# Optimization experiments

Measured on AMD Instinct MI355X. Metric: run time of the kernel, lower is better.

Reference implementation:

```python
import jax, jax.numpy as jnp
from jax import lax
import numpy as np

INPUT_DIM = 1024; ENT_DIM = 256; KEY_DIM = 32; FUNC_DIM = 256; HID = 32
NUM_LAYERS = 1; UNIT_TYPE_DIM = 259; MAX_ENT = 64; B = 256; N = 512
NEG = 1e9

def _ln(x, g, b, eps=1e-5):
    m = x.mean(-1, keepdims=True)
    v = ((x - m) ** 2).mean(-1, keepdims=True)
    return (x - m) / jnp.sqrt(v + eps) * g + b

def setup_inputs() -> dict:
    key = jax.random.key(0)
    ks = jax.random.split(key, 16)
    def lin(k, i, o, s=0.02):
        return jax.random.normal(k, (i, o), jnp.float32) * s, jnp.zeros((o,), jnp.float32)
    p = {}
    p['key_fc_w'], p['key_fc_b'] = lin(ks[0], ENT_DIM, KEY_DIM)
    p['func_fc_w'], p['func_fc_b'] = lin(ks[1], UNIT_TYPE_DIM, FUNC_DIM)
    p['fc1_w'], p['fc1_b'] = lin(ks[2], INPUT_DIM, FUNC_DIM)
    p['fc2_w'], p['fc2_b'] = lin(ks[3], FUNC_DIM, KEY_DIM)
    p['embed_fc_w'], p['embed_fc_b'] = lin(ks[4], KEY_DIM, INPUT_DIM)
    p['lstm_wx'] = jax.random.normal(ks[5], (NUM_LAYERS, KEY_DIM, 4 * HID), jnp.float32) * 0.05
    p['lstm_wh'] = jax.random.normal(ks[6], (NUM_LAYERS, HID, 4 * HID), jnp.float32) * 0.05
    p['lstm_b'] = jnp.zeros((NUM_LAYERS, 4 * HID), jnp.float32)
    p['lstm_ln_gx'] = jnp.ones((NUM_LAYERS, 4 * HID), jnp.float32)
    p['lstm_ln_bx'] = jnp.zeros((NUM_LAYERS, 4 * HID), jnp.float32)
    p['lstm_ln_gh'] = jnp.ones((NUM_LAYERS, 4 * HID), jnp.float32)
    p['lstm_ln_bh'] = jnp.zeros((NUM_LAYERS, 4 * HID), jnp.float32)
    inp = {
        'embedding': jax.random.normal(ks[7], (B, INPUT_DIM), jnp.float32),
        'available_unit_type_mask': (jax.random.uniform(ks[8], (B, UNIT_TYPE_DIM)) < 0.5).astype(jnp.float32),
        'available_units_mask': jnp.ones((B, N), jnp.float32),
        'entity_embedding': jax.random.normal(ks[9], (B, N, ENT_DIM), jnp.float32),
        'temperature': jnp.float32(1.0),
    }
    inp.update(p)
    return inp

def reference(embedding, available_unit_type_mask, available_units_mask, entity_embedding,
              temperature, key_fc_w, key_fc_b, func_fc_w, func_fc_b, fc1_w, fc1_b,
              fc2_w, fc2_b, embed_fc_w, embed_fc_b, lstm_wx, lstm_wh, lstm_b,
              lstm_ln_gx, lstm_ln_bx, lstm_ln_gh, lstm_ln_bh):
    relu = jax.nn.relu
    # _get_key: [B,N,KEY] + end-flag row of zeros -> [B,N+1,KEY]
    key = entity_embedding @ key_fc_w + key_fc_b
    key = jnp.concatenate([key, jnp.zeros((B, 1, KEY_DIM), key.dtype)], axis=1)
    end_idx = N
    # _get_init_query
    func_embed = relu(available_unit_type_mask @ func_fc_w + func_fc_b)
    x0 = relu(embedding @ fc1_w + fc1_b)
    x0 = relu((x0 + func_embed) @ fc2_w + fc2_b)  # [B, KEY_DIM]
    mask0 = jnp.concatenate([available_units_mask, jnp.ones((B, 1), available_units_mask.dtype)], axis=1)

    h0 = jnp.zeros((NUM_LAYERS, B, HID), key.dtype)
    c0 = jnp.zeros((NUM_LAYERS, B, HID), key.dtype)
    units0 = jnp.zeros((B, N + 1), jnp.int32)
    done0 = jnp.zeros((B,), bool)
    rng0 = jax.random.key(42)

    def step(carry, _):
        x, h, c, mask, units, done, rng = carry
        xi = x
        hs, cs = [], []
        for l in range(NUM_LAYERS):  # LN-LSTM, gate order i,f,o,u (DI-engine)
            gate = (_ln(xi @ lstm_wx[l], lstm_ln_gx[l], lstm_ln_bx[l])
                    + _ln(h[l] @ lstm_wh[l], lstm_ln_gh[l], lstm_ln_bh[l]) + lstm_b[l])
            i_g, f_g, o_g, u_g = jnp.split(gate, 4, axis=-1)
            cl = jax.nn.sigmoid(f_g) * c[l] + jax.nn.sigmoid(i_g) * jnp.tanh(u_g)
            hl = jax.nn.sigmoid(o_g) * jnp.tanh(cl)
            hs.append(hl); cs.append(cl); xi = hl
        h_new = jnp.stack(hs); c_new = jnp.stack(cs)
        q = (xi[:, None, :] * key).mean(-1)          # [B, N+1] pointer scores
        q = q - (1.0 - mask) * NEG
        rng, sk = jax.random.split(rng)
        idx = jax.random.categorical(sk, q / temperature, axis=-1)  # [B]
        is_end = idx == end_idx
        active = jnp.logical_not(done)
        sel = active & jnp.logical_not(is_end)
        onehot = jax.nn.one_hot(idx, N + 1, dtype=mask.dtype)
        units = jnp.where(sel[:, None] & (onehot > 0.5), 1, units)
        mask = jnp.where(sel[:, None], mask * (1.0 - onehot), mask)
        done = done | (active & is_end)
        return (xi, h_new, c_new, mask, units, done, rng), (q, active)

    carry, (logits, valid) = lax.scan(step, (x0, h0, c0, mask0, units0, done0, rng0), None, length=MAX_ENT)
    units = carry[4]
    emb_sel = (units[..., None].astype(key.dtype) * key).mean(axis=1)  # [B, KEY_DIM]
    emb_sel = emb_sel @ embed_fc_w + embed_fc_b
    return logits, valid, units, embedding + emb_sel
```

## Files before the change

### kernel.cpp

```cpp
#include <hip/hip_runtime.h>
#include <stdint.h>
#include <stddef.h>

#define JAX_PARTITIONABLE 1

#define B_   256
#define N_   512
#define NP_  513
#define KROW 516
#define T_   64
#define CS   4
#define NCH  16
#define NEGC 1e9f

__host__ __device__ __forceinline__ void tf2x32(uint32_t k0, uint32_t k1,
    uint32_t x0, uint32_t x1, uint32_t& o0, uint32_t& o1) {
  const uint32_t k2 = k0 ^ k1 ^ 0x1BD11BDAu;
#define TFR(r) { x0 += x1; x1 = (x1 << (r)) | (x1 >> (32 - (r))); x1 ^= x0; }
  x0 += k0; x1 += k1;
  TFR(13) TFR(15) TFR(26) TFR(6)
  x0 += k1; x1 += k2 + 1u;
  TFR(17) TFR(29) TFR(16) TFR(24)
  x0 += k2; x1 += k0 + 2u;
  TFR(13) TFR(15) TFR(26) TFR(6)
  x0 += k0; x1 += k1 + 3u;
  TFR(17) TFR(29) TFR(16) TFR(24)
  x0 += k1; x1 += k2 + 4u;
  TFR(13) TFR(15) TFR(26) TFR(6)
  x0 += k2; x1 += k0 + 5u;
#undef TFR
  o0 = x0; o1 = x1;
}

struct SkKeys { uint32_t k[128]; };

static SkKeys compute_chain() {
  SkKeys s;
  uint32_t r0 = 0u, r1 = 42u;
  for (int t = 0; t < 64; ++t) {
#if JAX_PARTITIONABLE
    uint32_t a0, a1, b0, b1;
    tf2x32(r0, r1, 0u, 0u, a0, a1);
    tf2x32(r0, r1, 0u, 1u, b0, b1);
    s.k[2*t] = b0; s.k[2*t+1] = b1;
    r0 = a0; r1 = a1;
#else
    uint32_t p0, p1, q0, q1;
    tf2x32(r0, r1, 0u, 2u, p0, p1);
    tf2x32(r0, r1, 1u, 3u, q0, q1);
    s.k[2*t] = p1; s.k[2*t+1] = q1;
    r0 = p0; r1 = q0;
#endif
  }
  return s;
}

__device__ __forceinline__ float gumbel_draw(uint32_t k0, uint32_t k1, int b, int n) {
  uint32_t bits;
#if JAX_PARTITIONABLE
  uint32_t j = (uint32_t)(b * NP_ + n);
  uint32_t o0, o1; tf2x32(k0, k1, 0u, j, o0, o1);
  bits = o0 ^ o1;
#else
  int j = b * NP_ + n;
  uint32_t o0, o1;
  if (j < 65664) { tf2x32(k0, k1, (uint32_t)j, (uint32_t)(j + 65664), o0, o1); bits = o0; }
  else           { tf2x32(k0, k1, (uint32_t)(j - 65664), (uint32_t)j, o0, o1); bits = o1; }
#endif
  float f = __uint_as_float((bits >> 9) | 0x3F800000u) - 1.0f;
  const float TINY = 1.17549435e-38f;
  float u = fmaxf(TINY, f + TINY);
  return -logf(-logf(u));
}

__device__ __forceinline__ float sigm(float x) {
  return 0.5f + 0.5f * tanhf(0.5f * x);
}

__device__ __forceinline__ void bar_lds() {
  asm volatile("s_waitcnt lgkmcnt(0)\n\ts_barrier" ::: "memory");
}

#define WS_KEY 0
#define WS_X0  (B_ * 32 * KROW)

__global__ void __launch_bounds__(256)
pre_kernel(const float* __restrict__ ent, const float* __restrict__ key_w,
           const float* __restrict__ key_b,
           const float* __restrict__ emb, const float* __restrict__ fc1_w,
           const float* __restrict__ fc1_b,
           const float* __restrict__ autm, const float* __restrict__ func_w,
           const float* __restrict__ func_b,
           const float* __restrict__ fc2_w, const float* __restrict__ fc2_b,
           float* __restrict__ ws)
{
  __shared__ __align__(16) float smAll[16384];
  const int tid = threadIdx.x;

  if (blockIdx.x < 1024) {
    float* smA = smAll;
    float* smW = smAll + 8192;
    const int blk = blockIdx.x;
    const int R0  = blk * 128;
    const int b   = R0 >> 9;
    const int nb  = R0 & 511;
    const int rg  = tid >> 3;
    const int cg  = tid & 7;

    for (int i = tid; i < 2048; i += 256)
      ((float4*)smW)[i] = ((const float4*)key_w)[i];

    float acc[4][4];
    #pragma unroll
    for (int i = 0; i < 4; ++i)
      #pragma unroll
      for (int j = 0; j < 4; ++j) acc[i][j] = 0.f;

    const int row  = tid >> 1;
    const int half = tid & 1;

    for (int kc = 0; kc < 4; ++kc) {
      const float4* src = (const float4*)(ent + ((size_t)(R0 + row)) * 256 + kc * 64 + half * 32);
      float4 vv[8];
      #pragma unroll
      for (int r = 0; r < 8; ++r) vv[r] = src[r];
      #pragma unroll
      for (int r = 0; r < 8; ++r) {
        const int kl = half * 32 + r * 4;
        smA[(kl + 0) * 128 + row] = vv[r].x;
        smA[(kl + 1) * 128 + row] = vv[r].y;
        smA[(kl + 2) * 128 + row] = vv[r].z;
        smA[(kl + 3) * 128 + row] = vv[r].w;
      }
      __syncthreads();
      #pragma unroll 4
      for (int k = 0; k < 64; ++k) {
        float4 av = *(const float4*)&smA[k * 128 + rg * 4];
        float4 bv = *(const float4*)&smW[(kc * 64 + k) * 32 + cg * 4];
        float ar[4] = {av.x, av.y, av.z, av.w};
        float br[4] = {bv.x, bv.y, bv.z, bv.w};
        #pragma unroll
        for (int i = 0; i < 4; ++i)
          #pragma unroll
          for (int j = 0; j < 4; ++j) acc[i][j] += ar[i] * br[j];
      }
      __syncthreads();
    }
    float4 bb = *(const float4*)&key_b[cg * 4];
    float bbr[4] = {bb.x, bb.y, bb.z, bb.w};
    #pragma unroll
    for (int j = 0; j < 4; ++j) {
      const int c = cg * 4 + j;
      float* dst = ws + WS_KEY + ((size_t)(b * 32 + c)) * KROW + nb + rg * 4;
      #pragma unroll
      for (int i = 0; i < 4; ++i) dst[i] = acc[i][j] + bbr[j];
    }
  } else {
    float* smX = smAll;
    const int b = blockIdx.x - 1024;
    const int j = tid;
    {
      float a = 0.f;
      const float* e = emb + (size_t)b * 1024;
      #pragma unroll 8
      for (int k = 0; k < 1024; ++k) a += e[k] * fc1_w[k * 256 + j];
      a = fmaxf(a + fc1_b[j], 0.f);
      float f = 0.f;
      const float* m = autm + (size_t)b * 259;
      for (int k = 0; k < 259; ++k) f += m[k] * func_w[k * 256 + j];
      f = fmaxf(f + func_b[j], 0.f);
      smX[j] = a + f;
    }
    __syncthreads();
    if (j < 32) {
      float s = 0.f;
      #pragma unroll 8
      for (int m = 0; m < 256; ++m) s += smX[m] * fc2_w[m * 32 + j];
      ws[WS_X0 + b * 32 + j] = fmaxf(s + fc2_b[j], 0.f);
    }
  }
}

#define OFF_KEY   0
#define OFF_H     16512
#define OFF_Q     18560
#define OFF_G     22688
#define OFF_UNITS 26816
#define OFF_SK    27332
#define OFF_ES    27460
#define OFF_PART  27492
#define LDS_FLOATS 28004

__global__ void __launch_bounds__(512, 2)
suh_kernel(const float* __restrict__ ws_key_x0,
           const float* __restrict__ aum, const float* __restrict__ temp_p,
           const float* __restrict__ emb,
           const float* __restrict__ emb_w, const float* __restrict__ emb_b,
           const float* __restrict__ wx, const float* __restrict__ wh,
           const float* __restrict__ lstm_bb,
           const float* __restrict__ ln_gx, const float* __restrict__ ln_bx,
           const float* __restrict__ ln_gh, const float* __restrict__ ln_bh,
           float* __restrict__ out_logits, float* __restrict__ out_valid,
           float* __restrict__ out_units, float* __restrict__ out_final,
           SkKeys sk)
{
  extern __shared__ __align__(16) float sm[];
  int* smi = (int*)sm;
  const int b   = blockIdx.x;
  const int tid = threadIdx.x;

  {
    const float4* kv = (const float4*)(ws_key_x0 + WS_KEY + (size_t)b * (32 * KROW));
    for (int i = tid; i < (32 * KROW) / 4; i += 512) ((float4*)sm)[i] = kv[i];
  }
  if (tid < 128) smi[OFF_SK + tid] = (int)sk.k[tid];
  __syncthreads();
  if (tid < 32) sm[OFF_KEY + tid * KROW + N_] = 0.f;

  const float temp = temp_p[0];

  float mreg[8], ureg[8];
  float m512 = 1.0f;
  int done_reg = 0;

  if (tid < 64) {
    float wxr0[32], wxr1[32], whr0[32], whr1[32];
    #pragma unroll
    for (int k = 0; k < 32; ++k) {
      wxr0[k] = wx[k * 128 + tid];
      wxr1[k] = wx[k * 128 + 64 + tid];
      whr0[k] = wh[k * 128 + tid];
      whr1[k] = wh[k * 128 + 64 + tid];
    }
    const float gxg0 = ln_gx[tid], gxg1 = ln_gx[tid + 64];
    const float gxb0 = ln_bx[tid], gxb1 = ln_bx[tid + 64];
    const float ghg0 = ln_gh[tid], ghg1 = ln_gh[tid + 64];
    const float ghb0 = ln_bh[tid], ghb1 = ln_bh[tid + 64];
    const float lb0  = lstm_bb[tid], lb1 = lstm_bb[tid + 64];

    float xfrag[32];
    {
      const float* x0g = ws_key_x0 + WS_X0 + b * 32;
      #pragma unroll
      for (int r = 0; r < 8; ++r) {
        float4 v = *(const float4*)(x0g + r * 4);
        xfrag[r*4] = v.x; xfrag[r*4+1] = v.y; xfrag[r*4+2] = v.z; xfrag[r*4+3] = v.w;
      }
    }
    float creg = 0.f;

    #pragma unroll 1
    for (int t = 0; t < T_; ++t) {
      float a0 = 0.f, a1 = 0.f, b0 = 0.f, b1 = 0.f;
      #pragma unroll
      for (int k = 0; k < 32; ++k) {
        a0 += xfrag[k] * wxr0[k];
        a1 += xfrag[k] * wxr1[k];
      }
      if (t > 0) {
        #pragma unroll
        for (int k = 0; k < 32; ++k) {
          b0 += xfrag[k] * whr0[k];
          b1 += xfrag[k] * whr1[k];
        }
      }
      float sx = a0 + a1, sh = b0 + b1;
      for (int off = 32; off; off >>= 1) {
        sx += __shfl_down(sx, off);
        sh += __shfl_down(sh, off);
      }
      float mx  = __shfl(sx, 0) * (1.0f / 128.0f);
      float mhh = __shfl(sh, 0) * (1.0f / 128.0f);
      float dx0 = a0 - mx, dx1 = a1 - mx;
      float dh0 = b0 - mhh, dh1 = b1 - mhh;
      float ssx = dx0 * dx0 + dx1 * dx1;
      float ssh = dh0 * dh0 + dh1 * dh1;
      for (int off = 32; off; off >>= 1) {
        ssx += __shfl_down(ssx, off);
        ssh += __shfl_down(ssh, off);
      }
      float vx = __shfl(ssx, 0) * (1.0f / 128.0f);
      float vh = __shfl(ssh, 0) * (1.0f / 128.0f);
      float rx = 1.0f / sqrtf(vx + 1e-5f);
      float rh = 1.0f / sqrtf(vh + 1e-5f);
      float lnx0 = dx0 * rx * gxg0 + gxb0;
      float lnx1 = dx1 * rx * gxg1 + gxb1;
      float lnh0 = dh0 * rh * ghg0 + ghb0;
      float lnh1 = dh1 * rh * ghg1 + ghb1;
      float g0 = lnx0 + lnh0 + lb0;
      float g1 = lnx1 + lnh1 + lb1;
      float fq = __shfl(g0, tid + 32);
      float uq = __shfl(g1, tid + 32);
      if (tid < 32) {
        float cN = sigm(fq) * creg + sigm(g0) * tanhf(uq);
        float hN = sigm(g1) * tanhf(cN);
        creg = cN;
        sm[OFF_H + t * 32 + tid] = hN;
      }
      #pragma unroll
      for (int r = 0; r < 8; ++r) {
        float4 v = *(const float4*)&sm[OFF_H + t * 32 + r * 4];
        xfrag[r*4] = v.x; xfrag[r*4+1] = v.y; xfrag[r*4+2] = v.z; xfrag[r*4+3] = v.w;
      }
    }
  }
  __syncthreads();

  auto do_prep = [&](int cc, int pbuf) {
    const int L = tid - 64;
    const int qb = OFF_Q + pbuf * (CS * 516);
    const int gb = OFF_G + pbuf * (CS * 516);
    #pragma unroll 1
    for (int pass = 0; pass < 2; ++pass) {
      const int n = L + pass * 448;
      if (pass == 0 || L < 65) {
        float kreg[32];
        #pragma unroll
        for (int k = 0; k < 32; ++k) kreg[k] = sm[OFF_KEY + k * KROW + n];
        #pragma unroll
        for (int tl = 0; tl < CS; ++tl) {
          float acc = 0.f;
          #pragma unroll
          for (int k = 0; k < 32; ++k) acc += sm[OFF_H + (cc * CS + tl) * 32 + k] * kreg[k];
          sm[qb + tl * 516 + n] = acc * (1.0f / 32.0f);
        }
      }
    }
    #pragma unroll 1
    for (int i = 0; i < (CS * 512 + 447) / 448; ++i) {
      const int idx = i * 448 + L;
      if (idx < CS * 512) {
        const int tl = idx >> 9;
        const int n  = idx & 511;
        const int t  = cc * CS + tl;
        sm[gb + tl * 516 + n] =
            gumbel_draw((uint32_t)smi[OFF_SK + 2*t], (uint32_t)smi[OFF_SK + 2*t + 1], b, n);
      }
    }
    if (L < CS) {
      const int t = cc * CS + L;
      sm[gb + L * 516 + N_] =
          gumbel_draw((uint32_t)smi[OFF_SK + 2*t], (uint32_t)smi[OFF_SK + 2*t + 1], b, N_);
    }
  };

  if (tid >= 64) {
    do_prep(0, 0);
  } else {
    #pragma unroll
    for (int j = 0; j < 8; ++j) {
      const int n = tid + 64 * j;
      mreg[j] = aum[(size_t)b * N_ + n];
      ureg[j] = 0.f;
    }
  }
  bar_lds();

  for (int c = 0; c < NCH; ++c) {
    const int pb = c & 1;
    if (tid < 64) {
      const int qbase = OFF_Q + pb * (CS * 516);
      const int gbase = OFF_G + pb * (CS * 516);
      #pragma unroll 1
      for (int tl = 0; tl < CS; ++tl) {
        const int t = c * CS + tl;
        float* lrow = out_logits + ((size_t)t * B_ + b) * NP_;
        float bv = 0.f; int bi = 0;
        #pragma unroll
        for (int j = 0; j < 8; ++j) {
          const int n = tid + 64 * j;
          float q = sm[qbase + tl * 516 + n] - (1.0f - mreg[j]) * NEGC;
          lrow[n] = q;
          float v = q / temp + sm[gbase + tl * 516 + n];
          if (j == 0) { bv = v; bi = n; }
          else if (v > bv) { bv = v; bi = n; }
        }
        if (tid == 0) {
          float q = -(1.0f - m512) * NEGC;
          lrow[N_] = q;
          float v = q / temp + sm[gbase + tl * 516 + N_];
          if (v > bv) { bv = v; bi = N_; }
        }
        for (int off = 32; off; off >>= 1) {
          float ov = __shfl_down(bv, off);
          int   oi = __shfl_down(bi, off);
          if (ov > bv || (ov == bv && oi < bi)) { bv = ov; bi = oi; }
        }
        const int sel_i = __shfl(bi, 0);
        const int active = !done_reg;
        const int is_end = (sel_i == N_);
        if (tid == 0) out_valid[(size_t)t * B_ + b] = active ? 1.0f : 0.0f;
        if (active && !is_end) {
          #pragma unroll
          for (int j = 0; j < 8; ++j)
            if (tid + 64 * j == sel_i) { mreg[j] = 0.0f; ureg[j] = 1.0f; }
        }
        if (active && is_end) done_reg = 1;
      }
    } else if (c + 1 < NCH) {
      do_prep(c + 1, (c + 1) & 1);
    }
    bar_lds();
  }

  if (tid < 64) {
    #pragma unroll
    for (int j = 0; j < 8; ++j) sm[OFF_UNITS + tid + 64 * j] = ureg[j];
    if (tid == 0) sm[OFF_UNITS + N_] = 0.f;
  }
  __syncthreads();

  {
    const int g = tid >> 5, cc = tid & 31;
    float p = 0.f;
    const int n0 = g * 32;
    for (int nn = 0; nn < 32; ++nn) {
      const int n = n0 + nn;
      p += sm[OFF_UNITS + n] * sm[OFF_KEY + cc * KROW + n];
    }
    if (g == 15) p += sm[OFF_UNITS + N_] * sm[OFF_KEY + cc * KROW + N_];
    sm[OFF_PART + g * 32 + cc] = p;
  }
  for (int n = tid; n < NP_; n += 512) out_units[(size_t)b * NP_ + n] = sm[OFF_UNITS + n];
  __syncthreads();
  if (tid < 32) {
    float s = 0.f;
    #pragma unroll
    for (int g = 0; g < 16; ++g) s += sm[OFF_PART + g * 32 + tid];
    sm[OFF_ES + tid] = s / 513.0f;
  }
  __syncthreads();
  {
    const float* e = emb + (size_t)b * 1024;
    for (int d = tid; d < 1024; d += 512) {
      float a = 0.f;
      #pragma unroll
      for (int k = 0; k < 32; ++k) a += sm[OFF_ES + k] * emb_w[k * 1024 + d];
      out_final[(size_t)b * 1024 + d] = e[d] + a + emb_b[d];
    }
  }
}

extern "C" void kernel_launch(void* const* d_in, const int* in_sizes, int n_in,
                              void* d_out, int out_size, void* d_ws, size_t ws_size,
                              hipStream_t stream) {
  (void)in_sizes; (void)n_in; (void)ws_size; (void)out_size;
  const float* emb    = (const float*)d_in[0];
  const float* autm   = (const float*)d_in[1];
  const float* aum    = (const float*)d_in[2];
  const float* ent    = (const float*)d_in[3];
  const float* temp   = (const float*)d_in[4];
  const float* key_w  = (const float*)d_in[5];
  const float* key_b  = (const float*)d_in[6];
  const float* func_w = (const float*)d_in[7];
  const float* func_b = (const float*)d_in[8];
  const float* fc1_w  = (const float*)d_in[9];
  const float* fc1_b  = (const float*)d_in[10];
  const float* fc2_w  = (const float*)d_in[11];
  const float* fc2_b  = (const float*)d_in[12];
  const float* emb_w  = (const float*)d_in[13];
  const float* emb_b  = (const float*)d_in[14];
  const float* wx     = (const float*)d_in[15];
  const float* wh     = (const float*)d_in[16];
  const float* lb     = (const float*)d_in[17];
  const float* gxg    = (const float*)d_in[18];
  const float* gxb    = (const float*)d_in[19];
  const float* ghg    = (const float*)d_in[20];
  const float* ghb    = (const float*)d_in[21];
  float* out = (float*)d_out;
  float* ws  = (float*)d_ws;

  const size_t OFF_V = (size_t)T_ * B_ * NP_;
  const size_t OFF_U = OFF_V + (size_t)T_ * B_;
  const size_t OFF_F = OFF_U + (size_t)B_ * NP_;

  SkKeys sk = compute_chain();

  pre_kernel<<<dim3(1280), dim3(256), 0, stream>>>(
      ent, key_w, key_b, emb, fc1_w, fc1_b, autm, func_w, func_b,
      fc2_w, fc2_b, ws);

  suh_kernel<<<dim3(B_), dim3(512), LDS_FLOATS * sizeof(float), stream>>>(
      ws, aum, temp, emb, emb_w, emb_b,
      wx, wh, lb, gxg, gxb, ghg, ghb,
      out, out + OFF_V, out + OFF_U, out + OFF_F, sk);
}
```

Measured before the change: 275.4 us.

## Fuse key projection and MLP prologue into single per-batch pointer kernel

Removes the separate pre_kernel and computes the entity key projection, fc1/func/fc2 MLP and x0 inside the main per-batch kernel, overlapping the key GEMM with the LSTM recurrence on the first 64 threads. Each prep thread keeps its key columns in registers (kr0/kr1) so q computation reads h from LDS instead of reloading keys, and gumbel buffers are expanded to five slots so draws are prefetched several chunks ahead. The LSTM now broadcasts h via shuffles instead of an LDS round trip. It drops the workspace round trip and a launch but puts the key GEMM on 256 blocks with per-thread uncoalesced row reads, and raises register and LDS pressure.

```diff
diff --git a/kernel.cpp b/kernel.cpp
--- a/kernel.cpp
+++ b/kernel.cpp
@@ -81,147 +81,114 @@
   asm volatile("s_waitcnt lgkmcnt(0)\n\ts_barrier" ::: "memory");
 }
 
-#define WS_KEY 0
-#define WS_X0  (B_ * 32 * KROW)
-
-__global__ void __launch_bounds__(256)
-pre_kernel(const float* __restrict__ ent, const float* __restrict__ key_w,
-           const float* __restrict__ key_b,
-           const float* __restrict__ emb, const float* __restrict__ fc1_w,
-           const float* __restrict__ fc1_b,
-           const float* __restrict__ autm, const float* __restrict__ func_w,
-           const float* __restrict__ func_b,
-           const float* __restrict__ fc2_w, const float* __restrict__ fc2_b,
-           float* __restrict__ ws)
-{
-  __shared__ __align__(16) float smAll[16384];
-  const int tid = threadIdx.x;
-
-  if (blockIdx.x < 1024) {
-    float* smA = smAll;
-    float* smW = smAll + 8192;
-    const int blk = blockIdx.x;
-    const int R0  = blk * 128;
-    const int b   = R0 >> 9;
-    const int nb  = R0 & 511;
-    const int rg  = tid >> 3;
-    const int cg  = tid & 7;
-
-    for (int i = tid; i < 2048; i += 256)
-      ((float4*)smW)[i] = ((const float4*)key_w)[i];
-
-    float acc[4][4];
-    #pragma unroll
-    for (int i = 0; i < 4; ++i)
-      #pragma unroll
-      for (int j = 0; j < 4; ++j) acc[i][j] = 0.f;
-
-    const int row  = tid >> 1;
-    const int half = tid & 1;
-
-    for (int kc = 0; kc < 4; ++kc) {
-      const float4* src = (const float4*)(ent + ((size_t)(R0 + row)) * 256 + kc * 64 + half * 32);
-      float4 vv[8];
-      #pragma unroll
-      for (int r = 0; r < 8; ++r) vv[r] = src[r];
-      #pragma unroll
-      for (int r = 0; r < 8; ++r) {
-        const int kl = half * 32 + r * 4;
-        smA[(kl + 0) * 128 + row] = vv[r].x;
-        smA[(kl + 1) * 128 + row] = vv[r].y;
-        smA[(kl + 2) * 128 + row] = vv[r].z;
-        smA[(kl + 3) * 128 + row] = vv[r].w;
-      }
-      __syncthreads();
-      #pragma unroll 4
-      for (int k = 0; k < 64; ++k) {
-        float4 av = *(const float4*)&smA[k * 128 + rg * 4];
-        float4 bv = *(const float4*)&smW[(kc * 64 + k) * 32 + cg * 4];
-        float ar[4] = {av.x, av.y, av.z, av.w};
-        float br[4] = {bv.x, bv.y, bv.z, bv.w};
-        #pragma unroll
-        for (int i = 0; i < 4; ++i)
-          #pragma unroll
-          for (int j = 0; j < 4; ++j) acc[i][j] += ar[i] * br[j];
-      }
-      __syncthreads();
-    }
-    float4 bb = *(const float4*)&key_b[cg * 4];
-    float bbr[4] = {bb.x, bb.y, bb.z, bb.w};
-    #pragma unroll
-    for (int j = 0; j < 4; ++j) {
-      const int c = cg * 4 + j;
-      float* dst = ws + WS_KEY + ((size_t)(b * 32 + c)) * KROW + nb + rg * 4;
-      #pragma unroll
-      for (int i = 0; i < 4; ++i) dst[i] = acc[i][j] + bbr[j];
-    }
-  } else {
-    float* smX = smAll;
-    const int b = blockIdx.x - 1024;
-    const int j = tid;
-    {
-      float a = 0.f;
-      const float* e = emb + (size_t)b * 1024;
-      #pragma unroll 8
-      for (int k = 0; k < 1024; ++k) a += e[k] * fc1_w[k * 256 + j];
-      a = fmaxf(a + fc1_b[j], 0.f);
-      float f = 0.f;
-      const float* m = autm + (size_t)b * 259;
-      for (int k = 0; k < 259; ++k) f += m[k] * func_w[k * 256 + j];
-      f = fmaxf(f + func_b[j], 0.f);
-      smX[j] = a + f;
-    }
-    __syncthreads();
-    if (j < 32) {
-      float s = 0.f;
-      #pragma unroll 8
-      for (int m = 0; m < 256; ++m) s += smX[m] * fc2_w[m * 32 + j];
-      ws[WS_X0 + b * 32 + j] = fmaxf(s + fc2_b[j], 0.f);
-    }
-  }
-}
-
 #define OFF_KEY   0
 #define OFF_H     16512
 #define OFF_Q     18560
 #define OFF_G     22688
-#define OFF_UNITS 26816
-#define OFF_SK    27332
-#define OFF_ES    27460
-#define OFF_PART  27492
-#define LDS_FLOATS 28004
+#define OFF_UNITS 33008
+#define OFF_SK    33524
+#define OFF_ES    33652
+#define OFF_PART  33684
+#define OFF_T     34196
+#define OFF_X0    34452
+#define LDS_FLOATS 34484
 
 __global__ void __launch_bounds__(512, 2)
-suh_kernel(const float* __restrict__ ws_key_x0,
-           const float* __restrict__ aum, const float* __restrict__ temp_p,
-           const float* __restrict__ emb,
-           const float* __restrict__ emb_w, const float* __restrict__ emb_b,
-           const float* __restrict__ wx, const float* __restrict__ wh,
-           const float* __restrict__ lstm_bb,
-           const float* __restrict__ ln_gx, const float* __restrict__ ln_bx,
-           const float* __restrict__ ln_gh, const float* __restrict__ ln_bh,
-           float* __restrict__ out_logits, float* __restrict__ out_valid,
-           float* __restrict__ out_units, float* __restrict__ out_final,
-           SkKeys sk)
+suh_fused(const float* __restrict__ emb, const float* __restrict__ autm,
+          const float* __restrict__ aum, const float* __restrict__ ent,
+          const float* __restrict__ temp_p,
+          const float* __restrict__ key_w, const float* __restrict__ key_b,
+          const float* __restrict__ func_w, const float* __restrict__ func_b,
+          const float* __restrict__ fc1_w, const float* __restrict__ fc1_b,
+          const float* __restrict__ fc2_w, const float* __restrict__ fc2_b,
+          const float* __restrict__ emb_w, const float* __restrict__ emb_b,
+          const float* __restrict__ wx, const float* __restrict__ wh,
+          const float* __restrict__ lstm_bb,
+          const float* __restrict__ ln_gx, const float* __restrict__ ln_bx,
+          const float* __restrict__ ln_gh, const float* __restrict__ ln_bh,
+          float* __restrict__ out_logits, float* __restrict__ out_valid,
+          float* __restrict__ out_units, float* __restrict__ out_final,
+          SkKeys sk)
 {
   extern __shared__ __align__(16) float sm[];
   int* smi = (int*)sm;
   const int b   = blockIdx.x;
   const int tid = threadIdx.x;
-
-  {
-    const float4* kv = (const float4*)(ws_key_x0 + WS_KEY + (size_t)b * (32 * KROW));
-    for (int i = tid; i < (32 * KROW) / 4; i += 512) ((float4*)sm)[i] = kv[i];
-  }
-  if (tid < 128) smi[OFF_SK + tid] = (int)sk.k[tid];
-  __syncthreads();
-  if (tid < 32) sm[OFF_KEY + tid * KROW + N_] = 0.f;
+  const int L   = tid - 64;
 
   const float temp = temp_p[0];
 
+  if (tid < 256) {
+    float a = 0.f;
+    const float* e = emb + (size_t)b * 1024;
+    #pragma unroll 8
+    for (int k = 0; k < 1024; ++k) a += e[k] * fc1_w[k * 256 + tid];
+    a = fmaxf(a + fc1_b[tid], 0.f);
+    float f = 0.f;
+    const float* m = autm + (size_t)b * 259;
+    for (int k = 0; k < 259; ++k) f += m[k] * func_w[k * 256 + tid];
+    f = fmaxf(f + func_b[tid], 0.f);
+    sm[OFF_T + tid] = a + f;
+  } else {
+    if (tid < 384) smi[OFF_SK + (tid - 256)] = (int)sk.k[tid - 256];
+    if (tid >= 480) sm[OFF_KEY + (tid - 480) * KROW + N_] = 0.f;
+  }
+  __syncthreads();
+
+  if (tid < 32) {
+    float s = 0.f;
+    #pragma unroll 8
+    for (int m2 = 0; m2 < 256; ++m2) s += sm[OFF_T + m2] * fc2_w[m2 * 32 + tid];
+    sm[OFF_X0 + tid] = fmaxf(s + fc2_b[tid], 0.f);
+  }
+  __syncthreads();
+
+  float kr0[32], kr1[32];
   float mreg[8], ureg[8];
   float m512 = 1.0f;
   int done_reg = 0;
+
+  auto qprep = [&](int cc, int qs) {
+    const int qb = OFF_Q + qs * (CS * 516);
+    #pragma unroll 1
+    for (int tl = 0; tl < CS; ++tl) {
+      const int hb = OFF_H + (cc * CS + tl) * 32;
+      float hv[32];
+      #pragma unroll
+      for (int r = 0; r < 8; ++r) {
+        float4 v = *(const float4*)&sm[hb + r * 4];
+        hv[r*4] = v.x; hv[r*4+1] = v.y; hv[r*4+2] = v.z; hv[r*4+3] = v.w;
+      }
+      float a0 = 0.f;
+      #pragma unroll
+      for (int k = 0; k < 32; ++k) a0 += hv[k] * kr0[k];
+      sm[qb + tl * 516 + L] = a0 * (1.0f / 32.0f);
+      if (L < 64) {
+        float a1 = 0.f;
+        #pragma unroll
+        for (int k = 0; k < 32; ++k) a1 += hv[k] * kr1[k];
+        sm[qb + tl * 516 + L + 448] = a1 * (1.0f / 32.0f);
+      }
+    }
+  };
+  auto gprep = [&](int cc, int gs) {
+    const int gb = OFF_G + gs * (CS * 516);
+    #pragma unroll 1
+    for (int i = 0; i < 5; ++i) {
+      const int idx = i * 448 + L;
+      if (idx < CS * 512) {
+        const int tl = idx >> 9, n = idx & 511;
+        const int t = cc * CS + tl;
+        sm[gb + tl * 516 + n] =
+            gumbel_draw((uint32_t)smi[OFF_SK + 2*t], (uint32_t)smi[OFF_SK + 2*t + 1], b, n);
+      }
+    }
+    if (L < CS) {
+      const int t = cc * CS + L;
+      sm[gb + L * 516 + N_] =
+          gumbel_draw((uint32_t)smi[OFF_SK + 2*t], (uint32_t)smi[OFF_SK + 2*t + 1], b, N_);
+    }
+  };
 
   if (tid < 64) {
     float wxr0[32], wxr1[32], whr0[32], whr1[32];
@@ -232,20 +199,21 @@
       whr0[k] = wh[k * 128 + tid];
       whr1[k] = wh[k * 128 + 64 + tid];
     }
+    #pragma unroll
+    for (int k = 0; k < 32; ++k) {
+      asm volatile("" : "+v"(wxr0[k]), "+v"(wxr1[k]), "+v"(whr0[k]), "+v"(whr1[k]));
+    }
     const float gxg0 = ln_gx[tid], gxg1 = ln_gx[tid + 64];
     const float gxb0 = ln_bx[tid], gxb1 = ln_bx[tid + 64];
     const float ghg0 = ln_gh[tid], ghg1 = ln_gh[tid + 64];
     const float ghb0 = ln_bh[tid], ghb1 = ln_bh[tid + 64];
     const float lb0  = lstm_bb[tid], lb1 = lstm_bb[tid + 64];
 
-    float xfrag[32];
-    {
-      const float* x0g = ws_key_x0 + WS_X0 + b * 32;
-      #pragma unroll
-      for (int r = 0; r < 8; ++r) {
-        float4 v = *(const float4*)(x0g + r * 4);
-        xfrag[r*4] = v.x; xfrag[r*4+1] = v.y; xfrag[r*4+2] = v.z; xfrag[r*4+3] = v.w;
-      }
+    float xf[32];
+    #pragma unroll
+    for (int r = 0; r < 8; ++r) {
+      float4 v = *(const float4*)&sm[OFF_X0 + r * 4];
+      xf[r*4] = v.x; xf[r*4+1] = v.y; xf[r*4+2] = v.z; xf[r*4+3] = v.w;
     }
     float creg = 0.f;
 
@@ -253,16 +221,10 @@
     for (int t = 0; t < T_; ++t) {
       float a0 = 0.f, a1 = 0.f, b0 = 0.f, b1 = 0.f;
       #pragma unroll
-      for (int k = 0; k < 32; ++k) {
-        a0 += xfrag[k] * wxr0[k];
-        a1 += xfrag[k] * wxr1[k];
-      }
+      for (int k = 0; k < 32; ++k) { a0 += xf[k] * wxr0[k]; a1 += xf[k] * wxr1[k]; }
       if (t > 0) {
         #pragma unroll
-        for (int k = 0; k < 32; ++k) {
-          b0 += xfrag[k] * whr0[k];
-          b1 += xfrag[k] * whr1[k];
-        }
+        for (int k = 0; k < 32; ++k) { b0 += xf[k] * whr0[k]; b1 += xf[k] * whr1[k]; }
       }
       float sx = a0 + a1, sh = b0 + b1;
       for (int off = 32; off; off >>= 1) {
@@ -270,9 +232,9 @@
         sh += __shfl_down(sh, off);
       }
       float mx  = __shfl(sx, 0) * (1.0f / 128.0f);
-      float mhh = __shfl(sh, 0) * (1.0f / 128.0f);
+      float mh2 = __shfl(sh, 0) * (1.0f / 128.0f);
       float dx0 = a0 - mx, dx1 = a1 - mx;
-      float dh0 = b0 - mhh, dh1 = b1 - mhh;
+      float dh0 = b0 - mh2, dh1 = b1 - mh2;
       float ssx = dx0 * dx0 + dx1 * dx1;
       float ssh = dh0 * dh0 + dh1 * dh1;
       for (int off = 32; off; off >>= 1) {
@@ -291,76 +253,96 @@
       float g1 = lnx1 + lnh1 + lb1;
       float fq = __shfl(g0, tid + 32);
       float uq = __shfl(g1, tid + 32);
-      if (tid < 32) {
-        float cN = sigm(fq) * creg + sigm(g0) * tanhf(uq);
-        float hN = sigm(g1) * tanhf(cN);
-        creg = cN;
-        sm[OFF_H + t * 32 + tid] = hN;
-      }
-      #pragma unroll
-      for (int r = 0; r < 8; ++r) {
-        float4 v = *(const float4*)&sm[OFF_H + t * 32 + r * 4];
-        xfrag[r*4] = v.x; xfrag[r*4+1] = v.y; xfrag[r*4+2] = v.z; xfrag[r*4+3] = v.w;
-      }
-    }
-  }
-  __syncthreads();
-
-  auto do_prep = [&](int cc, int pbuf) {
-    const int L = tid - 64;
-    const int qb = OFF_Q + pbuf * (CS * 516);
-    const int gb = OFF_G + pbuf * (CS * 516);
+      float cN = sigm(fq) * creg + sigm(g0) * tanhf(uq);
+      float hN = sigm(g1) * tanhf(cN);
+      creg = cN;
+      if (tid < 32) sm[OFF_H + t * 32 + tid] = hN;
+      #pragma unroll
+      for (int k = 0; k < 32; ++k) xf[k] = __shfl(hN, k);
+    }
+  } else {
+    const float4* kw4 = (const float4*)key_w;
+    {
+      const float4* er = (const float4*)(ent + ((size_t)b * N_ + L) * 256);
+      float acc[32];
+      #pragma unroll
+      for (int c = 0; c < 32; ++c) acc[c] = 0.f;
+      #pragma unroll 1
+      for (int k4 = 0; k4 < 64; ++k4) {
+        float4 ev = er[k4];
+        float e4[4] = {ev.x, ev.y, ev.z, ev.w};
+        #pragma unroll
+        for (int j = 0; j < 4; ++j) {
+          const int k = k4 * 4 + j;
+          #pragma unroll
+          for (int c4 = 0; c4 < 8; ++c4) {
+            float4 w = kw4[k * 8 + c4];
+            acc[c4*4+0] += e4[j] * w.x;
+            acc[c4*4+1] += e4[j] * w.y;
+            acc[c4*4+2] += e4[j] * w.z;
+            acc[c4*4+3] += e4[j] * w.w;
+          }
+        }
+      }
+      #pragma unroll
+      for (int c = 0; c < 32; ++c) {
+        kr0[c] = acc[c] + key_b[c];
+        sm[OFF_KEY + c * KROW + L] = kr0[c];
+      }
+    }
+    if (L < 64) {
+      const int n = L + 448;
+      const float4* er = (const float4*)(ent + ((size_t)b * N_ + n) * 256);
+      float acc[32];
+      #pragma unroll
+      for (int c = 0; c < 32; ++c) acc[c] = 0.f;
+      #pragma unroll 1
+      for (int k4 = 0; k4 < 64; ++k4) {
+        float4 ev = er[k4];
+        float e4[4] = {ev.x, ev.y, ev.z, ev.w};
+        #pragma unroll
+        for (int j = 0; j < 4; ++j) {
+          const int k = k4 * 4 + j;
+          #pragma unroll
+          for (int c4 = 0; c4 < 8; ++c4) {
+            float4 w = kw4[k * 8 + c4];
+            acc[c4*4+0] += e4[j] * w.x;
+            acc[c4*4+1] += e4[j] * w.y;
+            acc[c4*4+2] += e4[j] * w.z;
+            acc[c4*4+3] += e4[j] * w.w;
+          }
+        }
+      }
+      #pragma unroll
+      for (int c = 0; c < 32; ++c) {
+        kr1[c] = acc[c] + key_b[c];
+        sm[OFF_KEY + c * KROW + n] = kr1[c];
+      }
+    }
+    #pragma unroll
+    for (int k = 0; k < 32; ++k) {
+      asm volatile("" : "+v"(kr0[k]), "+v"(kr1[k]));
+    }
     #pragma unroll 1
-    for (int pass = 0; pass < 2; ++pass) {
-      const int n = L + pass * 448;
-      if (pass == 0 || L < 65) {
-        float kreg[32];
-        #pragma unroll
-        for (int k = 0; k < 32; ++k) kreg[k] = sm[OFF_KEY + k * KROW + n];
-        #pragma unroll
-        for (int tl = 0; tl < CS; ++tl) {
-          float acc = 0.f;
-          #pragma unroll
-          for (int k = 0; k < 32; ++k) acc += sm[OFF_H + (cc * CS + tl) * 32 + k] * kreg[k];
-          sm[qb + tl * 516 + n] = acc * (1.0f / 32.0f);
-        }
-      }
-    }
-    #pragma unroll 1
-    for (int i = 0; i < (CS * 512 + 447) / 448; ++i) {
-      const int idx = i * 448 + L;
-      if (idx < CS * 512) {
-        const int tl = idx >> 9;
-        const int n  = idx & 511;
-        const int t  = cc * CS + tl;
-        sm[gb + tl * 516 + n] =
-            gumbel_draw((uint32_t)smi[OFF_SK + 2*t], (uint32_t)smi[OFF_SK + 2*t + 1], b, n);
-      }
-    }
-    if (L < CS) {
-      const int t = cc * CS + L;
-      sm[gb + L * 516 + N_] =
-          gumbel_draw((uint32_t)smi[OFF_SK + 2*t], (uint32_t)smi[OFF_SK + 2*t + 1], b, N_);
-    }
-  };
-
-  if (tid >= 64) {
-    do_prep(0, 0);
+    for (int cc = 0; cc < 4; ++cc) gprep(cc, cc);
+  }
+  __syncthreads();
+
+  if (tid < 64) {
+    #pragma unroll
+    for (int j = 0; j < 8; ++j) {
+      mreg[j] = aum[(size_t)b * N_ + tid + 64 * j];
+      ureg[j] = 0.f;
+    }
   } else {
-    #pragma unroll
-    for (int j = 0; j < 8; ++j) {
-      const int n = tid + 64 * j;
-      mreg[j] = aum[(size_t)b * N_ + n];
-      ureg[j] = 0.f;
-    }
+    qprep(0, 0);
   }
   bar_lds();
 
   for (int c = 0; c < NCH; ++c) {
-    const int pb = c & 1;
     if (tid < 64) {
-      const int qbase = OFF_Q + pb * (CS * 516);
-      const int gbase = OFF_G + pb * (CS * 516);
+      const int qbase = OFF_Q + (c & 1) * (CS * 516);
+      const int gbase = OFF_G + (c % 5) * (CS * 516);
       #pragma unroll 1
       for (int tl = 0; tl < CS; ++tl) {
         const int t = c * CS + tl;
@@ -397,8 +379,9 @@
         }
         if (active && is_end) done_reg = 1;
       }
-    } else if (c + 1 < NCH) {
-      do_prep(c + 1, (c + 1) & 1);
+    } else {
+      if (c + 1 < NCH) qprep(c + 1, (c + 1) & 1);
+      if (c + 4 < NCH) gprep(c + 4, (c + 4) % 5);
     }
     bar_lds();
   }
@@ -444,7 +427,7 @@
 extern "C" void kernel_launch(void* const* d_in, const int* in_sizes, int n_in,
                               void* d_out, int out_size, void* d_ws, size_t ws_size,
                               hipStream_t stream) {
-  (void)in_sizes; (void)n_in; (void)ws_size; (void)out_size;
+  (void)in_sizes; (void)n_in; (void)d_ws; (void)ws_size; (void)out_size;
   const float* emb    = (const float*)d_in[0];
   const float* autm   = (const float*)d_in[1];
   const float* aum    = (const float*)d_in[2];
@@ -468,7 +451,6 @@
   const float* ghg    = (const float*)d_in[20];
   const float* ghb    = (const float*)d_in[21];
   float* out = (float*)d_out;
-  float* ws  = (float*)d_ws;
 
   const size_t OFF_V = (size_t)T_ * B_ * NP_;
   const size_t OFF_U = OFF_V + (size_t)T_ * B_;
@@ -476,12 +458,9 @@
 
   SkKeys sk = compute_chain();
 
-  pre_kernel<<<dim3(1280), dim3(256), 0, stream>>>(
-      ent, key_w, key_b, emb, fc1_w, fc1_b, autm, func_w, func_b,
-      fc2_w, fc2_b, ws);
-
-  suh_kernel<<<dim3(B_), dim3(512), LDS_FLOATS * sizeof(float), stream>>>(
-      ws, aum, temp, emb, emb_w, emb_b,
+  suh_fused<<<dim3(B_), dim3(512), LDS_FLOATS * sizeof(float), stream>>>(
+      emb, autm, aum, ent, temp, key_w, key_b, func_w, func_b,
+      fc1_w, fc1_b, fc2_w, fc2_b, emb_w, emb_b,
       wx, wh, lb, gxg, gxb, ghg, ghb,
       out, out + OFF_V, out + OFF_U, out + OFF_F, sk);
 }
```

Result: faster. 242.4 us (-12.0%).
